# Kernel tuning notes

Measured on AMD Instinct MI355X. Metric: run time of the kernel, lower is better.

## Reference

```python
import jax, jax.numpy as jnp
import numpy as np

W_SIM, W_REC, W_FREQ, W_IMP, W_TYPE = 0.45, 0.2, 0.15, 0.1, 0.1
TYPE_WEIGHT = 0.9
DECAY_HALF_LIFE = 200.0
TEMPERATURE = 0.07
LN_EPS = 1e-5


def _l2norm(v, axis=-1):
    # matches torch F.normalize (eps=1e-12 clamp on the norm)
    n = jnp.linalg.norm(v, axis=axis, keepdims=True)
    return v / jnp.maximum(n, 1e-12)


def setup_inputs() -> dict:
    key = jax.random.key(0)
    ks = jax.random.split(key, 8)
    B, D, S = 16384, 2048, 64
    s = 1.0 / np.sqrt(D)
    x = jax.random.normal(ks[0], (B, D), jnp.float32)
    prototypes = _l2norm(jax.random.normal(ks[1], (S, D), jnp.float32))
    proto_conf = jax.random.uniform(ks[2], (S,), jnp.float32)
    proto_age = jax.random.uniform(ks[3], (S,), jnp.float32)
    proto_evidence = jnp.ones((S,), jnp.float32)
    W_in = jax.random.normal(ks[4], (D, D), jnp.float32) * s
    b_in = jnp.zeros((D,), jnp.float32)
    Wr1 = jax.random.normal(ks[5], (D // 2, D), jnp.float32) * s
    br1 = jnp.zeros((D // 2,), jnp.float32)
    Wr2 = jax.random.normal(ks[6], (4, D // 2), jnp.float32) * (1.0 / np.sqrt(D // 2))
    br2 = jnp.zeros((4,), jnp.float32)
    W_out = jax.random.normal(ks[7], (D, 2 * D), jnp.float32) * (1.0 / np.sqrt(2 * D))
    b_out = jnp.zeros((D,), jnp.float32)
    ln_w = jnp.ones((D,), jnp.float32)
    ln_b = jnp.zeros((D,), jnp.float32)
    return {"x": x, "prototypes": prototypes, "proto_conf": proto_conf,
            "proto_age": proto_age, "proto_evidence": proto_evidence,
            "W_in": W_in, "b_in": b_in, "Wr1": Wr1, "br1": br1,
            "Wr2": Wr2, "br2": br2, "W_out": W_out, "b_out": b_out,
            "ln_w": ln_w, "ln_b": ln_b}


def reference(x, prototypes, proto_conf, proto_age, proto_evidence,
              W_in, b_in, Wr1, br1, Wr2, br2, W_out, b_out, ln_w, ln_b):
    S = prototypes.shape[0]
    protos_per_type = S // 4

    # in_proj + normalize
    h = x @ W_in.T + b_in                                  # [B, D]
    h_norm = _l2norm(h)

    # type router: Linear -> GELU(exact) -> Linear -> softmax
    r = jax.nn.gelu(x @ Wr1.T + br1, approximate=False)    # [B, D/2]
    type_weights = jax.nn.softmax(r @ Wr2.T + br2, axis=-1)  # [B, 4]

    # prototype similarity
    p_norm = _l2norm(prototypes)
    raw_sim = h_norm @ p_norm.T                            # [B, S]

    type_assign = jnp.arange(S) // protos_per_type         # [S] in {0..3}
    type_mask = type_weights[:, type_assign]               # [B, S]
    weighted_sim = raw_sim * type_mask * proto_conf[None, :]

    # multi-factor salience (fused elementwise)
    recency = jnp.exp(-proto_age / DECAY_HALF_LIFE)[None, :]
    freq_norm = (jnp.log(proto_evidence + 1.0) /
                 (jnp.log(proto_evidence.max() + 2.0) + 1e-8))[None, :]
    sal = (W_SIM * weighted_sim + W_REC * recency + W_FREQ * freq_norm
           + W_IMP * proto_conf[None, :] + W_TYPE * TYPE_WEIGHT)
    sal = jnp.clip(sal, 0.0, 1.0)

    # attention over prototype bank
    attn = jax.nn.softmax(sal / TEMPERATURE, axis=-1)       # [B, S]
    retrieved = attn @ prototypes                           # [B, D]

    combined = jnp.concatenate([x, retrieved], axis=-1)     # [B, 2D]
    out = jax.nn.gelu(combined @ W_out.T + b_out, approximate=False)
    # dropout is identity in eval mode

    # residual + LayerNorm (biased variance, eps=1e-5)
    y = out + x
    mu = jnp.mean(y, axis=-1, keepdims=True)
    var = jnp.mean((y - mu) ** 2, axis=-1, keepdims=True)
    return ln_w * (y - mu) / jnp.sqrt(var + LN_EPS) + ln_b
```

## Files before the change

kernel.cpp:

```cpp
#include <hip/hip_runtime.h>
#include <hip/hip_bf16.h>
#include <cstdint>

#define DEV __device__ __forceinline__

typedef __bf16 bf16x8 __attribute__((ext_vector_type(8)));
typedef float f32x4 __attribute__((ext_vector_type(4)));
typedef unsigned short ushort_t;
typedef ushort_t ushort8 __attribute__((ext_vector_type(8)));

DEV ushort_t f2bf(float f) {
  union { float f; uint32_t u; } x; x.f = f;
  uint32_t r = (x.u + 0x7fffu + ((x.u >> 16) & 1u)) >> 16;
  return (ushort_t)r;
}
DEV float bf2f(ushort_t b) {
  union { uint32_t u; float f; } x; x.u = ((uint32_t)b) << 16;
  return x.f;
}
DEV float gelu_exact(float v) {
  return 0.5f * v * (1.0f + erff(v * 0.70710678118654752f));
}
DEV void gload_lds16(const void* g, void* l) {
  __builtin_amdgcn_global_load_lds(
      (const __attribute__((address_space(1))) void*)g,
      (__attribute__((address_space(3))) void*)l, 16, 0, 0);
}
DEV void bar() {
  asm volatile("" ::: "memory");
  __builtin_amdgcn_s_barrier();
  asm volatile("" ::: "memory");
}
DEV void waitlgkm0() { asm volatile("s_waitcnt lgkmcnt(0)" ::: "memory"); }


__global__ __launch_bounds__(64) void prep_scal(
    const float* __restrict__ conf, const float* __restrict__ age,
    const float* __restrict__ ev, float* __restrict__ base, float* __restrict__ cs) {
  int l = threadIdx.x;
  float e = ev[l];
  float m = e;
  #pragma unroll
  for (int d = 1; d < 64; d <<= 1) m = fmaxf(m, __shfl_xor(m, d));
  float freq = logf(e + 1.f) / (logf(m + 2.f) + 1e-8f);
  base[l] = 0.2f * expf(-age[l] * (1.f / 200.f)) + 0.15f * freq + 0.1f * conf[l] + 0.09f;
  cs[l] = 0.45f * conf[l];
}

__global__ __launch_bounds__(256) void prep_pnorm(
    const float* __restrict__ protos, const float* __restrict__ b_in,
    float* __restrict__ p_norm, float* __restrict__ dvec) {
  const int s = blockIdx.x, t = threadIdx.x;
  const float* p = protos + (size_t)s * 2048;
  float vals[8];
  float ss = 0.f, sb = 0.f;
  #pragma unroll
  for (int ii = 0; ii < 2; ++ii) {
    float4 v = *(const float4*)(p + t * 8 + ii * 4);
    float4 bi = *(const float4*)(b_in + t * 8 + ii * 4);
    vals[ii * 4 + 0] = v.x; vals[ii * 4 + 1] = v.y; vals[ii * 4 + 2] = v.z; vals[ii * 4 + 3] = v.w;
    ss += v.x * v.x + v.y * v.y + v.z * v.z + v.w * v.w;
    sb += v.x * bi.x + v.y * bi.y + v.z * bi.z + v.w * bi.w;
  }
  #pragma unroll
  for (int d = 1; d < 64; d <<= 1) { ss += __shfl_xor(ss, d); sb += __shfl_xor(sb, d); }
  __shared__ float red[8];
  if ((t & 63) == 0) { red[t >> 6] = ss; red[4 + (t >> 6)] = sb; }
  __syncthreads();
  ss = red[0] + red[1] + red[2] + red[3];
  sb = red[4] + red[5] + red[6] + red[7];
  float inv = 1.f / fmaxf(sqrtf(ss), 1e-12f);
  #pragma unroll
  for (int k = 0; k < 8; ++k) p_norm[(size_t)s * 2048 + t * 8 + k] = vals[k] * inv;
  if (t == 0) dvec[s] = sb * inv;
}


__global__ __launch_bounds__(256) void conv_x(const float* __restrict__ x, ushort_t* __restrict__ xa) {
  size_t e = ((size_t)blockIdx.x * 256 + threadIdx.x) * 8;
  int row = (int)(e >> 11), col = (int)(e & 2047);
  float4 f0 = *(const float4*)(x + e);
  float4 f1 = *(const float4*)(x + e + 4);
  ushort8 o;
  o[0] = f2bf(f0.x); o[1] = f2bf(f0.y); o[2] = f2bf(f0.z); o[3] = f2bf(f0.w);
  o[4] = f2bf(f1.x); o[5] = f2bf(f1.y); o[6] = f2bf(f1.z); o[7] = f2bf(f1.w);
  *(ushort8*)(xa + (size_t)row * 2112 + col) = o;
}

__global__ __launch_bounds__(256) void conv_wbig(const float* __restrict__ W_in,
                                                 const float* __restrict__ Wr1,
                                                 ushort_t* __restrict__ wbig) {
  size_t e = ((size_t)blockIdx.x * 256 + threadIdx.x) * 8;
  int row = (int)(e >> 11), col = (int)(e & 2047);
  if (row >= 3072 && row < 3136) return;
  ushort8 o;
  if (row < 3072) {
    const float* src = (row < 2048) ? (W_in + (size_t)row * 2048 + col)
                                    : (Wr1 + (size_t)(row - 2048) * 2048 + col);
    float4 f0 = *(const float4*)(src);
    float4 f1 = *(const float4*)(src + 4);
    o[0] = f2bf(f0.x); o[1] = f2bf(f0.y); o[2] = f2bf(f0.z); o[3] = f2bf(f0.w);
    o[4] = f2bf(f1.x); o[5] = f2bf(f1.y); o[6] = f2bf(f1.z); o[7] = f2bf(f1.w);
  } else {
    o = ushort8{0, 0, 0, 0, 0, 0, 0, 0};
  }
  *(ushort8*)(wbig + (size_t)row * 2048 + col) = o;
}

__global__ __launch_bounds__(256) void conv_ww(const float* __restrict__ W_out,
                                               ushort_t* __restrict__ wwm) {
  size_t e = ((size_t)blockIdx.x * 256 + threadIdx.x) * 8;
  int n = (int)(e >> 11), c = (int)(e & 2047);
  float4 f0 = *(const float4*)(W_out + (size_t)n * 4096 + c);
  float4 f1 = *(const float4*)(W_out + (size_t)n * 4096 + c + 4);
  ushort8 o;
  o[0] = f2bf(f0.x); o[1] = f2bf(f0.y); o[2] = f2bf(f0.z); o[3] = f2bf(f0.w);
  o[4] = f2bf(f1.x); o[5] = f2bf(f1.y); o[6] = f2bf(f1.z); o[7] = f2bf(f1.w);
  *(ushort8*)(wwm + (size_t)n * 2112 + c) = o;
}

__global__ __launch_bounds__(256) void small_p2(const float* __restrict__ p_norm,
                                                const float* __restrict__ W_in,
                                                ushort_t* __restrict__ wbig) {
  __shared__ float pn[8][128];
  const int t = threadIdx.x;
  const int k = blockIdx.x * 128 + (t & 127);
  const int sh = t >> 7;
  const int s0 = blockIdx.y * 8;
  float acc[4] = {0.f, 0.f, 0.f, 0.f};
  for (int j0 = 0; j0 < 2048; j0 += 128) {
    __syncthreads();
    {
      int sl = t >> 5;
      int j4 = (t & 31) * 4;
      *(float4*)&pn[sl][j4] = *(const float4*)&p_norm[(size_t)(s0 + sl) * 2048 + j0 + j4];
    }
    __syncthreads();
    #pragma unroll 8
    for (int jj = 0; jj < 128; ++jj) {
      float wv = W_in[(size_t)(j0 + jj) * 2048 + k];
      #pragma unroll
      for (int i = 0; i < 4; ++i) acc[i] += pn[sh * 4 + i][jj] * wv;
    }
  }
  #pragma unroll
  for (int i = 0; i < 4; ++i)
    wbig[(size_t)(3072 + s0 + sh * 4 + i) * 2048 + k] = f2bf(acc[i]);
}

__global__ __launch_bounds__(256) void small_R(const float* __restrict__ protos,
                                               const float* __restrict__ W_out,
                                               ushort_t* __restrict__ wwm) {
  __shared__ float pch[64][68];
  __shared__ float wch[16][68];
  const int t = threadIdx.x;
  const int n_loc = t >> 4;
  const int sb = t & 15;
  const int n0 = blockIdx.x * 16;
  float acc[4] = {0.f, 0.f, 0.f, 0.f};
  for (int k0 = 0; k0 < 2048; k0 += 64) {
    __syncthreads();
    #pragma unroll
    for (int ii = 0; ii < 4; ++ii) {
      int lin4 = t * 4 + ii;
      int s = lin4 >> 4;
      int k4 = (lin4 & 15) * 4;
      *(float4*)&pch[s][k4] = *(const float4*)&protos[(size_t)s * 2048 + k0 + k4];
    }
    {
      int n_l = t >> 4;
      int k4 = (t & 15) * 4;
      *(float4*)&wch[n_l][k4] = *(const float4*)&W_out[(size_t)(n0 + n_l) * 4096 + 2048 + k0 + k4];
    }
    __syncthreads();
    #pragma unroll 8
    for (int kk = 0; kk < 64; ++kk) {
      float wv = wch[n_loc][kk];
      #pragma unroll
      for (int i = 0; i < 4; ++i) acc[i] += pch[sb + 16 * i][kk] * wv;
    }
  }
  #pragma unroll
  for (int i = 0; i < 4; ++i)
    wwm[(size_t)(n0 + n_loc) * 2112 + 2048 + sb + 16 * i] = f2bf(acc[i]);
}

template <int MODE>
__global__ __launch_bounds__(512, 2) void gemm256(
    const ushort_t* __restrict__ A, int lda,
    const ushort_t* __restrict__ Bw, int ldb, int K, int Brows,
    const float* __restrict__ bias0, const float* __restrict__ bias1,
    float* __restrict__ out0, ushort_t* __restrict__ out1, float* __restrict__ out2) {
  __shared__ char lds[131072];
  const int t = threadIdx.x;
  const int l = t & 63, w = t >> 6;
  const int wr = w >> 2, wc = w & 3;
  const int lr = l & 15, lg = l >> 4;
  const int bm = blockIdx.x * 256;
  const int bn = blockIdx.y * 256;
  const int NT = K >> 6;

  const int srow = t >> 3;
  const int schunk = t & 7;
  const int gsw = ((schunk ^ (srow & 7)) * 8);
  const int ldsL = srow * 128 + schunk * 16;

  char* const Ab = lds;
  char* const Bb = lds + 65536;

  auto stA = [&](int buf, int half, int kt) {
    const size_t gbase = (size_t)(bm + half * 128 + srow) * lda + (size_t)kt * 64 + gsw;
    char* const d = Ab + buf * 32768 + half * 16384 + ldsL;
    gload_lds16(A + gbase, d);
    gload_lds16(A + gbase + (size_t)64 * lda, d + 8192);
  };
  auto stB = [&](int buf, int half, int kt) {
    int r0 = bn + half * 128 + srow;
    int r1 = r0 + 64;
    if (r0 >= Brows) r0 = Brows - 1;
    if (r1 >= Brows) r1 = Brows - 1;
    const size_t koff = (size_t)kt * 64 + gsw;
    char* const d = Bb + buf * 32768 + half * 16384 + ldsL;
    gload_lds16(Bw + (size_t)r0 * ldb + koff, d);
    gload_lds16(Bw + (size_t)r1 * ldb + koff, d + 8192);
  };

  const int q16 = ((lg ^ (lr & 7)) << 4);
  const int laneA = (wr * 128 + lr) * 128 + q16;
  const int laneB = (wc * 64 + lr) * 128 + q16;

  f32x4 acc[8][4];
  #pragma unroll
  for (int i = 0; i < 8; ++i)
    #pragma unroll
    for (int j = 0; j < 4; ++j) acc[i][j] = f32x4{0.f, 0.f, 0.f, 0.f};

  stA(0, 0, 0); stA(0, 1, 0); stB(0, 0, 0); stB(0, 1, 0);
  stB(1, 0, 1); stB(1, 1, 1);
  asm volatile("s_waitcnt vmcnt(4)" ::: "memory");
  bar();

  bf16x8 av[4][2], b0v[2][2], b1v[2][2];

  for (int kt = 0; kt < NT; ++kt) {
    const int cur = kt & 1, nxt = cur ^ 1;
    const char* const Ac = Ab + cur * 32768;
    const char* const Bc = Bb + cur * 32768;

    #pragma unroll
    for (int i = 0; i < 4; ++i) {
      av[i][0] = *(const bf16x8*)(Ac + ((laneA + i * 2048) ^ 0));
      av[i][1] = *(const bf16x8*)(Ac + ((laneA + i * 2048) ^ 64));
    }
    #pragma unroll
    for (int j = 0; j < 2; ++j) {
      b0v[j][0] = *(const bf16x8*)(Bc + ((laneB + j * 2048) ^ 0));
      b0v[j][1] = *(const bf16x8*)(Bc + ((laneB + j * 2048) ^ 64));
    }
    if (kt + 1 < NT) stA(nxt, 0, kt + 1);
    bar();
    waitlgkm0();
    __builtin_amdgcn_s_setprio(1);
    #pragma unroll
    for (int i = 0; i < 4; ++i)
      #pragma unroll
      for (int j = 0; j < 2; ++j) {
        acc[i][j] = __builtin_amdgcn_mfma_f32_16x16x32_bf16(av[i][0], b0v[j][0], acc[i][j], 0, 0, 0);
        acc[i][j] = __builtin_amdgcn_mfma_f32_16x16x32_bf16(av[i][1], b0v[j][1], acc[i][j], 0, 0, 0);
      }
    __builtin_amdgcn_s_setprio(0);
    bar();

    #pragma unroll
    for (int j = 0; j < 2; ++j) {
      b1v[j][0] = *(const bf16x8*)(Bc + ((laneB + (2 + j) * 2048) ^ 0));
      b1v[j][1] = *(const bf16x8*)(Bc + ((laneB + (2 + j) * 2048) ^ 64));
    }
    if (kt + 1 < NT) stA(nxt, 1, kt + 1);
    bar();
    waitlgkm0();
    __builtin_amdgcn_s_setprio(1);
    #pragma unroll
    for (int i = 0; i < 4; ++i)
      #pragma unroll
      for (int j = 0; j < 2; ++j) {
        acc[i][2 + j] = __builtin_amdgcn_mfma_f32_16x16x32_bf16(av[i][0], b1v[j][0], acc[i][2 + j], 0, 0, 0);
        acc[i][2 + j] = __builtin_amdgcn_mfma_f32_16x16x32_bf16(av[i][1], b1v[j][1], acc[i][2 + j], 0, 0, 0);
      }
    __builtin_amdgcn_s_setprio(0);
    bar();

    #pragma unroll
    for (int i = 0; i < 4; ++i) {
      av[i][0] = *(const bf16x8*)(Ac + ((laneA + (4 + i) * 2048) ^ 0));
      av[i][1] = *(const bf16x8*)(Ac + ((laneA + (4 + i) * 2048) ^ 64));
    }
    if (kt + 2 < NT) stB(cur, 0, kt + 2);
    bar();
    waitlgkm0();
    __builtin_amdgcn_s_setprio(1);
    #pragma unroll
    for (int i = 0; i < 4; ++i)
      #pragma unroll
      for (int j = 0; j < 2; ++j) {
        acc[4 + i][2 + j] = __builtin_amdgcn_mfma_f32_16x16x32_bf16(av[i][0], b1v[j][0], acc[4 + i][2 + j], 0, 0, 0);
        acc[4 + i][2 + j] = __builtin_amdgcn_mfma_f32_16x16x32_bf16(av[i][1], b1v[j][1], acc[4 + i][2 + j], 0, 0, 0);
      }
    __builtin_amdgcn_s_setprio(0);
    bar();

    if (kt + 2 < NT) stB(cur, 1, kt + 2);
    bar();
    __builtin_amdgcn_s_setprio(1);
    #pragma unroll
    for (int i = 0; i < 4; ++i)
      #pragma unroll
      for (int j = 0; j < 2; ++j) {
        acc[4 + i][j] = __builtin_amdgcn_mfma_f32_16x16x32_bf16(av[i][0], b0v[j][0], acc[4 + i][j], 0, 0, 0);
        acc[4 + i][j] = __builtin_amdgcn_mfma_f32_16x16x32_bf16(av[i][1], b0v[j][1], acc[4 + i][j], 0, 0, 0);
      }
    __builtin_amdgcn_s_setprio(0);
    if (kt + 2 < NT) {
      asm volatile("s_waitcnt vmcnt(4)" ::: "memory");
    } else if (kt + 1 < NT) {
      asm volatile("s_waitcnt vmcnt(0)" ::: "memory");
    }
    bar();
  }

  if constexpr (MODE == 0) {
    #pragma unroll
    for (int i = 0; i < 8; ++i) {
      #pragma unroll
      for (int q = 0; q < 4; ++q) {
        const int grow = bm + wr * 128 + i * 16 + lg * 4 + q;
        if (bn < 2048) {
          float ss = 0.f;
          #pragma unroll
          for (int j = 0; j < 4; ++j) {
            const int gcol = bn + wc * 64 + j * 16 + lr;
            float v = acc[i][j][q] + bias0[gcol];
            ss += v * v;
          }
          ss += __shfl_xor(ss, 1);
          ss += __shfl_xor(ss, 2);
          ss += __shfl_xor(ss, 4);
          ss += __shfl_xor(ss, 8);
          if (lr == 0) atomicAdd(&out0[grow], ss);
        } else if (bn < 3072) {
          #pragma unroll
          for (int j = 0; j < 4; ++j) {
            const int gcol = bn + wc * 64 + j * 16 + lr;
            float v = acc[i][j][q] + bias1[gcol - 2048];
            out1[(size_t)grow * 1024 + (gcol - 2048)] = f2bf(gelu_exact(v));
          }
        } else {
          #pragma unroll
          for (int j = 0; j < 4; ++j) {
            const int gcol = bn + wc * 64 + j * 16 + lr;
            if (gcol < 3136) out2[(size_t)grow * 64 + (gcol - 3072)] = acc[i][j][q];
          }
        }
      }
    }
  } else {
    #pragma unroll
    for (int i = 0; i < 8; ++i)
      #pragma unroll
      for (int j = 0; j < 4; ++j)
        #pragma unroll
        for (int q = 0; q < 4; ++q) {
          const int grow = bm + wr * 128 + i * 16 + lg * 4 + q;
          const int gcol = bn + wc * 64 + j * 16 + lr;
          float v = acc[i][j][q] + bias0[gcol];
          float g = gelu_exact(v);
          out0[(size_t)grow * 2048 + gcol] = g + bias1[(size_t)grow * 2048 + gcol];
        }
  }
}

__global__ __launch_bounds__(256) void attn_k(
    const ushort_t* __restrict__ r_bf, const float* __restrict__ Wr2,
    const float* __restrict__ br2, const float* __restrict__ rn2,
    const float* __restrict__ rproj, const float* __restrict__ dvec,
    const float* __restrict__ base, const float* __restrict__ cs,
    ushort_t* __restrict__ xa) {
  const int b = blockIdx.x * 4 + (threadIdx.x >> 6);
  const int l = threadIdx.x & 63;
  const ushort_t* rrow = r_bf + (size_t)b * 1024;
  float t0 = 0.f, t1 = 0.f, t2 = 0.f, t3 = 0.f;
  #pragma unroll
  for (int m = 0; m < 16; ++m) {
    int k = l + m * 64;
    float rv = bf2f(rrow[k]);
    t0 += rv * Wr2[k];
    t1 += rv * Wr2[1024 + k];
    t2 += rv * Wr2[2048 + k];
    t3 += rv * Wr2[3072 + k];
  }
  #pragma unroll
  for (int d = 1; d < 64; d <<= 1) {
    t0 += __shfl_xor(t0, d); t1 += __shfl_xor(t1, d);
    t2 += __shfl_xor(t2, d); t3 += __shfl_xor(t3, d);
  }
  t0 += br2[0]; t1 += br2[1]; t2 += br2[2]; t3 += br2[3];
  float mx = fmaxf(fmaxf(t0, t1), fmaxf(t2, t3));
  float e0 = expf(t0 - mx), e1 = expf(t1 - mx), e2 = expf(t2 - mx), e3 = expf(t3 - mx);
  float sinv = 1.f / (e0 + e1 + e2 + e3);
  float tw0 = e0 * sinv, tw1 = e1 * sinv, tw2 = e2 * sinv, tw3 = e3 * sinv;
  const int ty = l >> 4;
  float twv = (ty == 0) ? tw0 : ((ty == 1) ? tw1 : ((ty == 2) ? tw2 : tw3));

  float inv = 1.f / fmaxf(sqrtf(rn2[b]), 1e-12f);
  float rp = rproj[(size_t)b * 64 + l] + dvec[l];
  float sal = cs[l] * twv * (rp * inv) + base[l];
  sal = fminf(fmaxf(sal, 0.f), 1.f);
  float logit = sal * (1.f / 0.07f);
  float lm = logit;
  #pragma unroll
  for (int d = 1; d < 64; d <<= 1) lm = fmaxf(lm, __shfl_xor(lm, d));
  float ex = expf(logit - lm);
  float es = ex;
  #pragma unroll
  for (int d = 1; d < 64; d <<= 1) es += __shfl_xor(es, d);
  float attn = ex / es;
  xa[(size_t)b * 2112 + 2048 + l] = f2bf(attn);
}

__global__ __launch_bounds__(256) void ln_k(float* __restrict__ y,
                                            const float* __restrict__ lw,
                                            const float* __restrict__ lb) {
  const int b = blockIdx.x, t = threadIdx.x;
  float* row = y + (size_t)b * 2048;
  float4 v0 = *(const float4*)(row + t * 8);
  float4 v1 = *(const float4*)(row + t * 8 + 4);
  float s = v0.x + v0.y + v0.z + v0.w + v1.x + v1.y + v1.z + v1.w;
  float s2 = v0.x * v0.x + v0.y * v0.y + v0.z * v0.z + v0.w * v0.w +
             v1.x * v1.x + v1.y * v1.y + v1.z * v1.z + v1.w * v1.w;
  #pragma unroll
  for (int d = 1; d < 64; d <<= 1) { s += __shfl_xor(s, d); s2 += __shfl_xor(s2, d); }
  __shared__ float red[8];
  if ((t & 63) == 0) { red[t >> 6] = s; red[4 + (t >> 6)] = s2; }
  __syncthreads();
  float ts = red[0] + red[1] + red[2] + red[3];
  float ts2 = red[4] + red[5] + red[6] + red[7];
  const float mu = ts * (1.f / 2048.f);
  const float inv = 1.f / sqrtf(ts2 * (1.f / 2048.f) - mu * mu + 1e-5f);
  float4 w0 = *(const float4*)(lw + t * 8), w1 = *(const float4*)(lw + t * 8 + 4);
  float4 b0 = *(const float4*)(lb + t * 8), b1 = *(const float4*)(lb + t * 8 + 4);
  float4 o0, o1;
  o0.x = (v0.x - mu) * inv * w0.x + b0.x;
  o0.y = (v0.y - mu) * inv * w0.y + b0.y;
  o0.z = (v0.z - mu) * inv * w0.z + b0.z;
  o0.w = (v0.w - mu) * inv * w0.w + b0.w;
  o1.x = (v1.x - mu) * inv * w1.x + b1.x;
  o1.y = (v1.y - mu) * inv * w1.y + b1.y;
  o1.z = (v1.z - mu) * inv * w1.z + b1.z;
  o1.w = (v1.w - mu) * inv * w1.w + b1.w;
  *(float4*)(row + t * 8) = o0;
  *(float4*)(row + t * 8 + 4) = o1;
}

extern "C" void kernel_launch(void* const* d_in, const int* in_sizes, int n_in,
                              void* d_out, int out_size, void* d_ws, size_t ws_size,
                              hipStream_t stream) {
  const float* x      = (const float*)d_in[0];
  const float* protos = (const float*)d_in[1];
  const float* conf   = (const float*)d_in[2];
  const float* age    = (const float*)d_in[3];
  const float* ev     = (const float*)d_in[4];
  const float* W_in   = (const float*)d_in[5];
  const float* b_in   = (const float*)d_in[6];
  const float* Wr1    = (const float*)d_in[7];
  const float* br1    = (const float*)d_in[8];
  const float* Wr2    = (const float*)d_in[9];
  const float* br2    = (const float*)d_in[10];
  const float* W_out  = (const float*)d_in[11];
  const float* b_out  = (const float*)d_in[12];
  const float* ln_w   = (const float*)d_in[13];
  const float* ln_b   = (const float*)d_in[14];
  float* out = (float*)d_out;

  char* ws = (char*)d_ws;
  size_t off = 0;
  auto take = [&](size_t bytes) {
    char* p = ws + off;
    off = (off + bytes + 255) & ~(size_t)255;
    return p;
  };
  ushort_t* xa    = (ushort_t*)take((size_t)16384 * 2112 * 2);
  ushort_t* wbig  = (ushort_t*)take((size_t)3200 * 2048 * 2);
  ushort_t* wwm   = (ushort_t*)take((size_t)2048 * 2112 * 2);
  ushort_t* rbf   = (ushort_t*)take((size_t)16384 * 1024 * 2);
  float*    rproj = (float*)take((size_t)16384 * 64 * 4);
  float*    rn2   = (float*)take((size_t)16384 * 4);
  float*    pnorm = (float*)take((size_t)64 * 2048 * 4);
  float*    base  = (float*)take(256);
  float*    cs    = (float*)take(256);
  float*    dvec  = (float*)take(256);
  (void)in_sizes; (void)n_in; (void)out_size; (void)ws_size;

  hipMemsetAsync(rn2, 0, 16384 * 4, stream);
  prep_scal<<<1, 64, 0, stream>>>(conf, age, ev, base, cs);
  prep_pnorm<<<64, 256, 0, stream>>>(protos, b_in, pnorm, dvec);
  conv_x<<<16384, 256, 0, stream>>>(x, xa);
  conv_wbig<<<3200, 256, 0, stream>>>(W_in, Wr1, wbig);
  conv_ww<<<2048, 256, 0, stream>>>(W_out, wwm);
  small_p2<<<dim3(16, 8), 256, 0, stream>>>(pnorm, W_in, wbig);
  small_R<<<128, 256, 0, stream>>>(protos, W_out, wwm);
  gemm256<0><<<dim3(64, 13), 512, 0, stream>>>(xa, 2112, wbig, 2048, 2048, 3200,
                                               b_in, br1, rn2, rbf, rproj);
  attn_k<<<4096, 256, 0, stream>>>(rbf, Wr2, br2, rn2, rproj, dvec, base, cs, xa);
  gemm256<1><<<dim3(64, 8), 512, 0, stream>>>(xa, 2112, wwm, 2112, 2112, 2048,
                                              b_out, x, out, nullptr, nullptr);
  ln_k<<<16384, 256, 0, stream>>>(out, ln_w, ln_b);
}
```

Baseline: 996.1 us.

## Unroll GEMM K-loop by two with static LDS buffers and pad K

The GEMM main loop now processes two K-tiles per iteration and uses four separately declared LDS arrays instead of one buffer indexed at runtime. This lets every load and store address be a compile-time constant, and the manual lgkmcnt(0) waits are dropped so the compiler can place finer-grained waits. To make the K-tile count even, the concatenated activation and weight matrices are padded from 2112 to 2176 columns, with the extra columns zero-filled. The cost is one extra zero K-tile of MFMA work and memory traffic in the output GEMM.

After: 1.027 ms. 3.1% more time.

```diff
diff --git a/kernel.cpp b/kernel.cpp
--- a/kernel.cpp
+++ b/kernel.cpp
@@ -31,7 +31,6 @@
   __builtin_amdgcn_s_barrier();
   asm volatile("" ::: "memory");
 }
-DEV void waitlgkm0() { asm volatile("s_waitcnt lgkmcnt(0)" ::: "memory"); }
 
 
 __global__ __launch_bounds__(64) void prep_scal(
@@ -75,16 +74,19 @@
   if (t == 0) dvec[s] = sb * inv;
 }
 
-
 __global__ __launch_bounds__(256) void conv_x(const float* __restrict__ x, ushort_t* __restrict__ xa) {
-  size_t e = ((size_t)blockIdx.x * 256 + threadIdx.x) * 8;
-  int row = (int)(e >> 11), col = (int)(e & 2047);
+  const int row = blockIdx.x, tid = threadIdx.x;
+  size_t e = (size_t)row * 2048 + tid * 8;
   float4 f0 = *(const float4*)(x + e);
   float4 f1 = *(const float4*)(x + e + 4);
   ushort8 o;
   o[0] = f2bf(f0.x); o[1] = f2bf(f0.y); o[2] = f2bf(f0.z); o[3] = f2bf(f0.w);
   o[4] = f2bf(f1.x); o[5] = f2bf(f1.y); o[6] = f2bf(f1.z); o[7] = f2bf(f1.w);
-  *(ushort8*)(xa + (size_t)row * 2112 + col) = o;
+  *(ushort8*)(xa + (size_t)row * 2176 + tid * 8) = o;
+  if (tid < 8) {
+    ushort8 z = ushort8{0, 0, 0, 0, 0, 0, 0, 0};
+    *(ushort8*)(xa + (size_t)row * 2176 + 2112 + tid * 8) = z;
+  }
 }
 
 __global__ __launch_bounds__(256) void conv_wbig(const float* __restrict__ W_in,
@@ -109,14 +111,17 @@
 
 __global__ __launch_bounds__(256) void conv_ww(const float* __restrict__ W_out,
                                                ushort_t* __restrict__ wwm) {
-  size_t e = ((size_t)blockIdx.x * 256 + threadIdx.x) * 8;
-  int n = (int)(e >> 11), c = (int)(e & 2047);
-  float4 f0 = *(const float4*)(W_out + (size_t)n * 4096 + c);
-  float4 f1 = *(const float4*)(W_out + (size_t)n * 4096 + c + 4);
+  const int n = blockIdx.x, tid = threadIdx.x;
+  float4 f0 = *(const float4*)(W_out + (size_t)n * 4096 + tid * 8);
+  float4 f1 = *(const float4*)(W_out + (size_t)n * 4096 + tid * 8 + 4);
   ushort8 o;
   o[0] = f2bf(f0.x); o[1] = f2bf(f0.y); o[2] = f2bf(f0.z); o[3] = f2bf(f0.w);
   o[4] = f2bf(f1.x); o[5] = f2bf(f1.y); o[6] = f2bf(f1.z); o[7] = f2bf(f1.w);
-  *(ushort8*)(wwm + (size_t)n * 2112 + c) = o;
+  *(ushort8*)(wwm + (size_t)n * 2176 + tid * 8) = o;
+  if (tid < 8) {
+    ushort8 z = ushort8{0, 0, 0, 0, 0, 0, 0, 0};
+    *(ushort8*)(wwm + (size_t)n * 2176 + 2112 + tid * 8) = z;
+  }
 }
 
 __global__ __launch_bounds__(256) void small_p2(const float* __restrict__ p_norm,
@@ -182,7 +187,7 @@
   }
   #pragma unroll
   for (int i = 0; i < 4; ++i)
-    wwm[(size_t)(n0 + n_loc) * 2112 + 2048 + sb + 16 * i] = f2bf(acc[i]);
+    wwm[(size_t)(n0 + n_loc) * 2176 + 2048 + sb + 16 * i] = f2bf(acc[i]);
 }
 
 template <int MODE>
@@ -191,7 +196,10 @@
     const ushort_t* __restrict__ Bw, int ldb, int K, int Brows,
     const float* __restrict__ bias0, const float* __restrict__ bias1,
     float* __restrict__ out0, ushort_t* __restrict__ out1, float* __restrict__ out2) {
-  __shared__ char lds[131072];
+  __shared__ __align__(16) ushort_t As0[16384];
+  __shared__ __align__(16) ushort_t As1[16384];
+  __shared__ __align__(16) ushort_t Bs0[16384];
+  __shared__ __align__(16) ushort_t Bs1[16384];
   const int t = threadIdx.x;
   const int l = t & 63, w = t >> 6;
   const int wr = w >> 2, wc = w & 3;
@@ -205,22 +213,23 @@
   const int gsw = ((schunk ^ (srow & 7)) * 8);
   const int ldsL = srow * 128 + schunk * 16;
 
-  char* const Ab = lds;
-  char* const Bb = lds + 65536;
-
-  auto stA = [&](int buf, int half, int kt) {
-    const size_t gbase = (size_t)(bm + half * 128 + srow) * lda + (size_t)kt * 64 + gsw;
-    char* const d = Ab + buf * 32768 + half * 16384 + ldsL;
-    gload_lds16(A + gbase, d);
-    gload_lds16(A + gbase + (size_t)64 * lda, d + 8192);
-  };
-  auto stB = [&](int buf, int half, int kt) {
+  auto stA = [&](ushort_t* dst, int kt) {
+    const size_t koff = (size_t)kt * 64 + gsw;
+    #pragma unroll
+    for (int h = 0; h < 2; ++h) {
+      const size_t g = (size_t)(bm + h * 128 + srow) * lda + koff;
+      char* d = (char*)dst + h * 16384 + ldsL;
+      gload_lds16(A + g, d);
+      gload_lds16(A + g + (size_t)64 * lda, d + 8192);
+    }
+  };
+  auto stBh = [&](ushort_t* dst, int half, int kt) {
     int r0 = bn + half * 128 + srow;
     int r1 = r0 + 64;
     if (r0 >= Brows) r0 = Brows - 1;
     if (r1 >= Brows) r1 = Brows - 1;
     const size_t koff = (size_t)kt * 64 + gsw;
-    char* const d = Bb + buf * 32768 + half * 16384 + ldsL;
+    char* const d = (char*)dst + half * 16384 + ldsL;
     gload_lds16(Bw + (size_t)r0 * ldb + koff, d);
     gload_lds16(Bw + (size_t)r1 * ldb + koff, d + 8192);
   };
@@ -235,96 +244,84 @@
     #pragma unroll
     for (int j = 0; j < 4; ++j) acc[i][j] = f32x4{0.f, 0.f, 0.f, 0.f};
 
-  stA(0, 0, 0); stA(0, 1, 0); stB(0, 0, 0); stB(0, 1, 0);
-  stB(1, 0, 1); stB(1, 1, 1);
-  asm volatile("s_waitcnt vmcnt(4)" ::: "memory");
-  bar();
-
   bf16x8 av[4][2], b0v[2][2], b1v[2][2];
-
-  for (int kt = 0; kt < NT; ++kt) {
-    const int cur = kt & 1, nxt = cur ^ 1;
-    const char* const Ac = Ab + cur * 32768;
-    const char* const Bc = Bb + cur * 32768;
-
+  auto rdA = [&](const ushort_t* src, int i0) {
     #pragma unroll
     for (int i = 0; i < 4; ++i) {
-      av[i][0] = *(const bf16x8*)(Ac + ((laneA + i * 2048) ^ 0));
-      av[i][1] = *(const bf16x8*)(Ac + ((laneA + i * 2048) ^ 64));
-    }
+      av[i][0] = *(const bf16x8*)((const char*)src + ((laneA + (i0 + i) * 2048)));
+      av[i][1] = *(const bf16x8*)((const char*)src + ((laneA + (i0 + i) * 2048) ^ 64));
+    }
+  };
+  auto rdB0 = [&](const ushort_t* src) {
     #pragma unroll
     for (int j = 0; j < 2; ++j) {
-      b0v[j][0] = *(const bf16x8*)(Bc + ((laneB + j * 2048) ^ 0));
-      b0v[j][1] = *(const bf16x8*)(Bc + ((laneB + j * 2048) ^ 64));
-    }
-    if (kt + 1 < NT) stA(nxt, 0, kt + 1);
-    bar();
-    waitlgkm0();
+      b0v[j][0] = *(const bf16x8*)((const char*)src + ((laneB + j * 2048)));
+      b0v[j][1] = *(const bf16x8*)((const char*)src + ((laneB + j * 2048) ^ 64));
+    }
+  };
+  auto rdB1 = [&](const ushort_t* src) {
+    #pragma unroll
+    for (int j = 0; j < 2; ++j) {
+      b1v[j][0] = *(const bf16x8*)((const char*)src + ((laneB + (2 + j) * 2048)));
+      b1v[j][1] = *(const bf16x8*)((const char*)src + ((laneB + (2 + j) * 2048) ^ 64));
+    }
+  };
+  auto mmB0 = [&](int i0) {
     __builtin_amdgcn_s_setprio(1);
     #pragma unroll
     for (int i = 0; i < 4; ++i)
       #pragma unroll
       for (int j = 0; j < 2; ++j) {
-        acc[i][j] = __builtin_amdgcn_mfma_f32_16x16x32_bf16(av[i][0], b0v[j][0], acc[i][j], 0, 0, 0);
-        acc[i][j] = __builtin_amdgcn_mfma_f32_16x16x32_bf16(av[i][1], b0v[j][1], acc[i][j], 0, 0, 0);
+        acc[i0 + i][j] = __builtin_amdgcn_mfma_f32_16x16x32_bf16(av[i][0], b0v[j][0], acc[i0 + i][j], 0, 0, 0);
+        acc[i0 + i][j] = __builtin_amdgcn_mfma_f32_16x16x32_bf16(av[i][1], b0v[j][1], acc[i0 + i][j], 0, 0, 0);
       }
     __builtin_amdgcn_s_setprio(0);
-    bar();
-
-    #pragma unroll
-    for (int j = 0; j < 2; ++j) {
-      b1v[j][0] = *(const bf16x8*)(Bc + ((laneB + (2 + j) * 2048) ^ 0));
-      b1v[j][1] = *(const bf16x8*)(Bc + ((laneB + (2 + j) * 2048) ^ 64));
-    }
-    if (kt + 1 < NT) stA(nxt, 1, kt + 1);
-    bar();
-    waitlgkm0();
+  };
+  auto mmB1 = [&](int i0) {
     __builtin_amdgcn_s_setprio(1);
     #pragma unroll
     for (int i = 0; i < 4; ++i)
       #pragma unroll
       for (int j = 0; j < 2; ++j) {
-        acc[i][2 + j] = __builtin_amdgcn_mfma_f32_16x16x32_bf16(av[i][0], b1v[j][0], acc[i][2 + j], 0, 0, 0);
-        acc[i][2 + j] = __builtin_amdgcn_mfma_f32_16x16x32_bf16(av[i][1], b1v[j][1], acc[i][2 + j], 0, 0, 0);
+        acc[i0 + i][2 + j] = __builtin_amdgcn_mfma_f32_16x16x32_bf16(av[i][0], b1v[j][0], acc[i0 + i][2 + j], 0, 0, 0);
+        acc[i0 + i][2 + j] = __builtin_amdgcn_mfma_f32_16x16x32_bf16(av[i][1], b1v[j][1], acc[i0 + i][2 + j], 0, 0, 0);
       }
     __builtin_amdgcn_s_setprio(0);
+  };
+
+  stA(As0, 0);
+  stBh(Bs0, 0, 0); stBh(Bs0, 1, 0);
+  stBh(Bs1, 0, 1); stBh(Bs1, 1, 1);
+  asm volatile("s_waitcnt vmcnt(4)" ::: "memory");
+  bar();
+
+  for (int it = 0, nit = NT >> 1; it < nit; ++it) {
+    const int U = it << 1;
+    const bool more = (U + 2) < NT;
+    rdA(As0, 0); rdB0(Bs0);
+    stA(As1, U + 1);
+    bar(); mmB0(0); bar();
+    rdB1(Bs0);
+    bar(); mmB1(0); bar();
+    rdA(As0, 4);
+    if (more) stBh(Bs0, 0, U + 2);
+    bar(); mmB1(4); bar();
+    if (more) stBh(Bs0, 1, U + 2);
+    bar(); mmB0(4);
+    if (more) { asm volatile("s_waitcnt vmcnt(4)" ::: "memory"); }
+    else      { asm volatile("s_waitcnt vmcnt(0)" ::: "memory"); }
     bar();
-
-    #pragma unroll
-    for (int i = 0; i < 4; ++i) {
-      av[i][0] = *(const bf16x8*)(Ac + ((laneA + (4 + i) * 2048) ^ 0));
-      av[i][1] = *(const bf16x8*)(Ac + ((laneA + (4 + i) * 2048) ^ 64));
-    }
-    if (kt + 2 < NT) stB(cur, 0, kt + 2);
-    bar();
-    waitlgkm0();
-    __builtin_amdgcn_s_setprio(1);
-    #pragma unroll
-    for (int i = 0; i < 4; ++i)
-      #pragma unroll
-      for (int j = 0; j < 2; ++j) {
-        acc[4 + i][2 + j] = __builtin_amdgcn_mfma_f32_16x16x32_bf16(av[i][0], b1v[j][0], acc[4 + i][2 + j], 0, 0, 0);
-        acc[4 + i][2 + j] = __builtin_amdgcn_mfma_f32_16x16x32_bf16(av[i][1], b1v[j][1], acc[4 + i][2 + j], 0, 0, 0);
-      }
-    __builtin_amdgcn_s_setprio(0);
-    bar();
-
-    if (kt + 2 < NT) stB(cur, 1, kt + 2);
-    bar();
-    __builtin_amdgcn_s_setprio(1);
-    #pragma unroll
-    for (int i = 0; i < 4; ++i)
-      #pragma unroll
-      for (int j = 0; j < 2; ++j) {
-        acc[4 + i][j] = __builtin_amdgcn_mfma_f32_16x16x32_bf16(av[i][0], b0v[j][0], acc[4 + i][j], 0, 0, 0);
-        acc[4 + i][j] = __builtin_amdgcn_mfma_f32_16x16x32_bf16(av[i][1], b0v[j][1], acc[4 + i][j], 0, 0, 0);
-      }
-    __builtin_amdgcn_s_setprio(0);
-    if (kt + 2 < NT) {
-      asm volatile("s_waitcnt vmcnt(4)" ::: "memory");
-    } else if (kt + 1 < NT) {
-      asm volatile("s_waitcnt vmcnt(0)" ::: "memory");
-    }
+    rdA(As1, 0); rdB0(Bs1);
+    if (more) stA(As0, U + 2);
+    bar(); mmB0(0); bar();
+    rdB1(Bs1);
+    bar(); mmB1(0); bar();
+    rdA(As1, 4);
+    if (more) stBh(Bs1, 0, U + 3);
+    bar(); mmB1(4); bar();
+    if (more) stBh(Bs1, 1, U + 3);
+    bar(); mmB0(4);
+    if (more) { asm volatile("s_waitcnt vmcnt(4)" ::: "memory"); }
     bar();
   }
 
@@ -424,7 +421,7 @@
   #pragma unroll
   for (int d = 1; d < 64; d <<= 1) es += __shfl_xor(es, d);
   float attn = ex / es;
-  xa[(size_t)b * 2112 + 2048 + l] = f2bf(attn);
+  xa[(size_t)b * 2176 + 2048 + l] = f2bf(attn);
 }
 
 __global__ __launch_bounds__(256) void ln_k(float* __restrict__ y,
@@ -488,9 +485,9 @@
     off = (off + bytes + 255) & ~(size_t)255;
     return p;
   };
-  ushort_t* xa    = (ushort_t*)take((size_t)16384 * 2112 * 2);
+  ushort_t* xa    = (ushort_t*)take((size_t)16384 * 2176 * 2);
   ushort_t* wbig  = (ushort_t*)take((size_t)3200 * 2048 * 2);
-  ushort_t* wwm   = (ushort_t*)take((size_t)2048 * 2112 * 2);
+  ushort_t* wwm   = (ushort_t*)take((size_t)2048 * 2176 * 2);
   ushort_t* rbf   = (ushort_t*)take((size_t)16384 * 1024 * 2);
   float*    rproj = (float*)take((size_t)16384 * 64 * 4);
   float*    rn2   = (float*)take((size_t)16384 * 4);
@@ -508,10 +505,10 @@
   conv_ww<<<2048, 256, 0, stream>>>(W_out, wwm);
   small_p2<<<dim3(16, 8), 256, 0, stream>>>(pnorm, W_in, wbig);
   small_R<<<128, 256, 0, stream>>>(protos, W_out, wwm);
-  gemm256<0><<<dim3(64, 13), 512, 0, stream>>>(xa, 2112, wbig, 2048, 2048, 3200,
+  gemm256<0><<<dim3(64, 13), 512, 0, stream>>>(xa, 2176, wbig, 2048, 2048, 3200,
                                                b_in, br1, rn2, rbf, rproj);
   attn_k<<<4096, 256, 0, stream>>>(rbf, Wr2, br2, rn2, rproj, dvec, base, cs, xa);
-  gemm256<1><<<dim3(64, 8), 512, 0, stream>>>(xa, 2112, wwm, 2112, 2112, 2048,
+  gemm256<1><<<dim3(64, 8), 512, 0, stream>>>(xa, 2176, wwm, 2176, 2176, 2048,
                                               b_out, x, out, nullptr, nullptr);
   ln_k<<<16384, 256, 0, stream>>>(out, ln_w, ln_b);
 }
```
